# Kernel optimization log

Hardware: AMD Instinct MI355X
Metric: run time of the kernel (lower is better)

The kernel has to match this reference:

```python
import jax, jax.numpy as jnp
import numpy as np

N = 50000          # nodes
E = 800000         # edges (avg degree 16)
INPUT_DIM = 1024
K = 10             # conv1d kernel
STRIDE = 8
COUT = (INPUT_DIM - K) // STRIDE + 1   # 127, matches floor formula
H = 256            # hidden_dim


def setup_inputs() -> dict:
    key = jax.random.key(0)
    ks = jax.random.split(key, 12)
    sc = lambda k, s: (jax.random.normal(k, s, jnp.float32) * 0.05)
    inp = {}
    inp["h"] = jax.random.normal(ks[0], (N, INPUT_DIM), jnp.float32)
    inp["src"] = jax.random.randint(ks[1], (E,), 0, N, dtype=jnp.int32)
    inp["dst"] = jax.random.randint(ks[2], (E,), 0, N, dtype=jnp.int32)
    # Conv1d(1,1,k=10,stride=8)
    inp["conv1d_w"] = sc(ks[3], (1, 1, K))
    inp["conv1d_b"] = jnp.zeros((1,), jnp.float32)
    # SAGEConv1: 127 -> 256 (mean aggregator: fc_self + fc_neigh)
    inp["w_self1"] = sc(ks[4], (COUT, H))
    inp["w_neigh1"] = sc(ks[5], (COUT, H))
    inp["b1"] = jnp.zeros((H,), jnp.float32)
    # SAGEConv2: 256 -> 128
    inp["w_self2"] = sc(ks[6], (H, H // 2))
    inp["w_neigh2"] = sc(ks[7], (H, H // 2))
    inp["b2"] = jnp.zeros((H // 2,), jnp.float32)
    # MLP head 128 -> 64 -> 32 -> 1
    inp["fc1_w"] = sc(ks[8], (H // 2, H // 4)); inp["fc1_b"] = jnp.zeros((H // 4,), jnp.float32)
    inp["fc2_w"] = sc(ks[9], (H // 4, H // 8)); inp["fc2_b"] = jnp.zeros((H // 8,), jnp.float32)
    inp["fc3_w"] = sc(ks[10], (H // 8, 1));    inp["fc3_b"] = jnp.zeros((1,), jnp.float32)
    return inp


def _sage_mean(x, src, dst, w_self, w_neigh, b):
    # mean over in-neighbors (src -> dst), zero for isolated nodes (DGL semantics)
    ones = jnp.ones((src.shape[0],), x.dtype)
    deg = jax.ops.segment_sum(ones, dst, num_segments=N)          # [N]
    agg = jax.ops.segment_sum(x[src], dst, num_segments=N)        # [N, F]
    agg = agg / jnp.maximum(deg, 1.0)[:, None]
    return x @ w_self + agg @ w_neigh + b


def reference(h, src, dst, conv1d_w, conv1d_b,
              w_self1, w_neigh1, b1, w_self2, w_neigh2, b2,
              fc1_w, fc1_b, fc2_w, fc2_b, fc3_w, fc3_b):
    # per-node 1D conv over feature axis: [N,1,1024] -> [N,1,127]
    x = jax.lax.conv_general_dilated(h[:, None, :], conv1d_w, (STRIDE,), 'VALID',
                                     dimension_numbers=('NCH', 'OIH', 'NCH'))
    x = jax.nn.relu(x[:, 0, :] + conv1d_b)                        # [N, 127]
    x = jax.nn.relu(_sage_mean(x, src, dst, w_self1, w_neigh1, b1))  # [N, 256]
    x = jax.nn.relu(_sage_mean(x, src, dst, w_self2, w_neigh2, b2))  # [N, 128]
    hg = jnp.mean(x, axis=0, keepdims=True)                       # AvgPooling -> [1, 128]
    y = jax.nn.relu(hg @ fc1_w + fc1_b)
    y = jax.nn.relu(y @ fc2_w + fc2_b)
    return y @ fc3_w + fc3_b                                      # [1, 1]
```

## Files before the change

kernel.cpp:

```cpp
#include <hip/hip_runtime.h>

#define N_NODES 50000
#define N_EDGES 800000
#define IN_DIM  1024
#define COUT    127
#define H1      256
#define H2      128
#define LDA     256
#define MBLK    391
#define EPB     2048
#define NROWS   8192
#define LDSS    72
#define EBLK    782
#define CVB     256

typedef __bf16 bf16;
typedef __attribute__((ext_vector_type(8))) __bf16 bf16x8;
typedef __attribute__((ext_vector_type(2))) __bf16 bf16x2;
typedef __attribute__((ext_vector_type(4))) float floatx4;

__device__ __forceinline__ float blo(unsigned int u) { return __uint_as_float(u << 16); }
__device__ __forceinline__ float bhi(unsigned int u) { return __uint_as_float(u & 0xffff0000u); }

__device__ __forceinline__ void conv_range(const float* __restrict__ h,
                                           const float* __restrict__ w, float bb,
                                           bf16* __restrict__ xa,
                                           int lo, int hi, int cb, int ncb) {
    int t   = threadIdx.x & 127;
    int sub = threadIdx.x >> 7;
    float wv[10];
    #pragma unroll
    for (int j = 0; j < 10; ++j) wv[j] = w[j];
    for (int n = lo + cb * 8 + sub; n < hi; n += ncb * 8) {
        const float* hr = h + (size_t)n * IN_DIM;
        float r = 0.f;
        if (t < COUT) {
            const float* q = hr + t * 8;
            float4 a = *(const float4*)q;
            float4 c = *(const float4*)(q + 4);
            float2 d = *(const float2*)(q + 8);
            float s = bb;
            s += a.x * wv[0] + a.y * wv[1] + a.z * wv[2] + a.w * wv[3];
            s += c.x * wv[4] + c.y * wv[5] + c.z * wv[6] + c.w * wv[7];
            s += d.x * wv[8] + d.y * wv[9];
            r = fmaxf(s, 0.f);
        }
        xa[(size_t)n * LDA + t] = (bf16)r;
    }
}

__global__ void padw_kernel(const float* __restrict__ ws1, const float* __restrict__ wn1,
                            const float* __restrict__ ws2, const float* __restrict__ wn2,
                            bf16* __restrict__ wt1, bf16* __restrict__ wt2,
                            int* __restrict__ deg) {
    int i = blockIdx.x * blockDim.x + threadIdx.x;
    int j = i & 65535;
    int n = j >> 8, k = j & 255;
    if (i < 65536) {
        float v = 0.f;
        if (k < COUT)                        v = ws1[k * H1 + n];
        else if (k >= 128 && k < 128 + COUT) v = wn1[(k - 128) * H1 + n];
        wt1[j] = (bf16)v;
    } else {
        float v = (n < H2) ? ws2[k * H2 + n] : wn2[k * H2 + (n - H2)];
        wt2[j] = (bf16)v;
    }
    if (i < 50048) deg[i] = 0;
}

__global__ __launch_bounds__(1024) void deg_conv_kernel(
        const int* __restrict__ dst, int* __restrict__ deg,
        const float* __restrict__ h, const float* __restrict__ cw,
        const float* __restrict__ cb, bf16* __restrict__ xa) {
    int bid = blockIdx.x;
    if (bid < EBLK) {
        int e = bid * 1024 + threadIdx.x;
        if (e < N_EDGES) atomicAdd(&deg[dst[e]], 1);
    } else {
        conv_range(h, cw, cb[0], xa, 0, 25000, bid - EBLK, CVB);
    }
}

__device__ void scan_block(const int* __restrict__ deg, int* __restrict__ rowptr,
                           int* __restrict__ cursor) {
    __shared__ int wsum[16];
    __shared__ int carry_s;
    int tid = threadIdx.x;
    int lane = tid & 63, wid = tid >> 6;
    if (tid == 0) carry_s = 0;
    __syncthreads();
    for (int base = 0; base < N_NODES; base += 8192) {
        int i0 = base + tid * 8;
        int v[8];
        if (i0 + 8 <= N_NODES) {
            int4 a = *(const int4*)&deg[i0];
            int4 c = *(const int4*)&deg[i0 + 4];
            v[0] = a.x; v[1] = a.y; v[2] = a.z; v[3] = a.w;
            v[4] = c.x; v[5] = c.y; v[6] = c.z; v[7] = c.w;
        } else {
            #pragma unroll
            for (int j = 0; j < 8; ++j) v[j] = (i0 + j < N_NODES) ? deg[i0 + j] : 0;
        }
        int p[8]; int run = 0;
        #pragma unroll
        for (int j = 0; j < 8; ++j) { run += v[j]; p[j] = run; }
        int s = run;
        #pragma unroll
        for (int off = 1; off < 64; off <<= 1) {
            int t = __shfl_up(s, off);
            if (lane >= off) s += t;
        }
        if (lane == 63) wsum[wid] = s;
        __syncthreads();
        if (tid < 16) {
            int ws = wsum[tid];
            #pragma unroll
            for (int off = 1; off < 16; off <<= 1) {
                int t = __shfl_up(ws, off);
                if (tid >= off) ws += t;
            }
            wsum[tid] = ws;
        }
        __syncthreads();
        int wpre  = (wid == 0) ? 0 : wsum[wid - 1];
        int excl0 = carry_s + wpre + (s - run);
        int o[8];
        #pragma unroll
        for (int j = 0; j < 8; ++j) o[j] = excl0 + p[j] - v[j];
        if (i0 + 8 <= N_NODES) {
            *(int4*)&rowptr[i0]     = make_int4(o[0], o[1], o[2], o[3]);
            *(int4*)&rowptr[i0 + 4] = make_int4(o[4], o[5], o[6], o[7]);
            *(int4*)&cursor[i0]     = make_int4(o[0], o[1], o[2], o[3]);
            *(int4*)&cursor[i0 + 4] = make_int4(o[4], o[5], o[6], o[7]);
        } else {
            for (int j = 0; j < 8; ++j)
                if (i0 + j < N_NODES) { rowptr[i0 + j] = o[j]; cursor[i0 + j] = o[j]; }
        }
        int tot = wsum[15];
        __syncthreads();
        if (tid == 0) carry_s += tot;
        __syncthreads();
    }
    if (tid == 0) rowptr[N_NODES] = carry_s;
}

__global__ __launch_bounds__(1024) void scan_conv_kernel(
        const int* __restrict__ deg, int* __restrict__ rowptr, int* __restrict__ cursor,
        const float* __restrict__ h, const float* __restrict__ cw,
        const float* __restrict__ cb, bf16* __restrict__ xa) {
    if (blockIdx.x == 0) {
        scan_block(deg, rowptr, cursor);
    } else {
        conv_range(h, cw, cb[0], xa, 25000, N_NODES, blockIdx.x - 1, CVB);
    }
}

__global__ __launch_bounds__(1024) void fill_kernel(
        const int* __restrict__ src, const int* __restrict__ dst,
        int* __restrict__ cursor, int* __restrict__ esrc) {
    int e = blockIdx.x * 1024 + threadIdx.x;
    if (e < N_EDGES) {
        int d = dst[e];
        int pos = atomicAdd(&cursor[d], 1);
        esrc[pos] = src[e];
    }
}

__global__ __launch_bounds__(256) void agg_kernel(bf16* __restrict__ xa,
                                                  const int* __restrict__ rowptr,
                                                  const int* __restrict__ esrc) {
    int lane = threadIdx.x & 63;
    int w    = threadIdx.x >> 6;
    int n    = blockIdx.x * 4 + w;
    int s0 = __builtin_amdgcn_readfirstlane(rowptr[n]);
    int s1 = __builtin_amdgcn_readfirstlane(rowptr[n + 1]);
    float ax = 0.f, ay = 0.f;
    int e = s0;
    for (; e + 8 <= s1; e += 8) {
        int i0 = esrc[e],     i1 = esrc[e + 1], i2 = esrc[e + 2], i3 = esrc[e + 3];
        int i4 = esrc[e + 4], i5 = esrc[e + 5], i6 = esrc[e + 6], i7 = esrc[e + 7];
        unsigned u0 = ((const unsigned*)(xa + (size_t)i0 * LDA))[lane];
        unsigned u1 = ((const unsigned*)(xa + (size_t)i1 * LDA))[lane];
        unsigned u2 = ((const unsigned*)(xa + (size_t)i2 * LDA))[lane];
        unsigned u3 = ((const unsigned*)(xa + (size_t)i3 * LDA))[lane];
        unsigned u4 = ((const unsigned*)(xa + (size_t)i4 * LDA))[lane];
        unsigned u5 = ((const unsigned*)(xa + (size_t)i5 * LDA))[lane];
        unsigned u6 = ((const unsigned*)(xa + (size_t)i6 * LDA))[lane];
        unsigned u7 = ((const unsigned*)(xa + (size_t)i7 * LDA))[lane];
        ax += ((blo(u0) + blo(u1)) + (blo(u2) + blo(u3)))
            + ((blo(u4) + blo(u5)) + (blo(u6) + blo(u7)));
        ay += ((bhi(u0) + bhi(u1)) + (bhi(u2) + bhi(u3)))
            + ((bhi(u4) + bhi(u5)) + (bhi(u6) + bhi(u7)));
    }
    for (; e < s1; ++e) {
        unsigned u = ((const unsigned*)(xa + (size_t)esrc[e] * LDA))[lane];
        ax += blo(u); ay += bhi(u);
    }
    float dnm = (float)max(s1 - s0, 1);
    bf16x2 o;
    o[0] = (bf16)(ax / dnm);
    o[1] = (bf16)(ay / dnm);
    *(bf16x2*)(xa + (size_t)n * LDA + 128 + 2 * lane) = o;
}

template <bool RELU>
__global__ __launch_bounds__(256) void gemm_mfma(
        const bf16* __restrict__ X, const bf16* __restrict__ WT,
        const float* __restrict__ bias, bf16* __restrict__ out) {
    __shared__ bf16 As[128 * LDSS];
    __shared__ bf16 Bs[64 * LDSS];
    int tid  = threadIdx.x;
    int lane = tid & 63, w = tid >> 6;
    int quad = lane >> 4, l16 = lane & 15;
    int m0 = blockIdx.x * 128;
    int n0 = blockIdx.y * 64;
    floatx4 acc[2][4] = {};

    for (int k0 = 0; k0 < 256; k0 += 64) {
        uint4 av[4], bv[2];
        #pragma unroll
        for (int i = 0; i < 4; ++i) {
            int c = tid + 256 * i;
            int row = c >> 3, col = (c & 7) * 8;
            int gr = m0 + row;
            av[i] = (gr < N_NODES) ? *(const uint4*)(X + (size_t)gr * LDA + k0 + col)
                                   : make_uint4(0u, 0u, 0u, 0u);
        }
        #pragma unroll
        for (int i = 0; i < 2; ++i) {
            int c = tid + 256 * i;
            int row = c >> 3, col = (c & 7) * 8;
            bv[i] = *(const uint4*)(WT + (size_t)(n0 + row) * 256 + k0 + col);
        }
        __syncthreads();
        #pragma unroll
        for (int i = 0; i < 4; ++i) {
            int c = tid + 256 * i;
            int row = c >> 3, col = (c & 7) * 8;
            *(uint4*)&As[row * LDSS + col] = av[i];
        }
        #pragma unroll
        for (int i = 0; i < 2; ++i) {
            int c = tid + 256 * i;
            int row = c >> 3, col = (c & 7) * 8;
            *(uint4*)&Bs[row * LDSS + col] = bv[i];
        }
        __syncthreads();

        #pragma unroll
        for (int ks = 0; ks < 2; ++ks) {
            int kin = ks * 32 + quad * 8;
            bf16x8 a0 = *(const bf16x8*)&As[(w * 32 + l16) * LDSS + kin];
            bf16x8 a1 = *(const bf16x8*)&As[(w * 32 + 16 + l16) * LDSS + kin];
            bf16x8 b0 = *(const bf16x8*)&Bs[(l16) * LDSS + kin];
            bf16x8 b1 = *(const bf16x8*)&Bs[(16 + l16) * LDSS + kin];
            bf16x8 b2 = *(const bf16x8*)&Bs[(32 + l16) * LDSS + kin];
            bf16x8 b3 = *(const bf16x8*)&Bs[(48 + l16) * LDSS + kin];
            acc[0][0] = __builtin_amdgcn_mfma_f32_16x16x32_bf16(a0, b0, acc[0][0], 0, 0, 0);
            acc[0][1] = __builtin_amdgcn_mfma_f32_16x16x32_bf16(a0, b1, acc[0][1], 0, 0, 0);
            acc[0][2] = __builtin_amdgcn_mfma_f32_16x16x32_bf16(a0, b2, acc[0][2], 0, 0, 0);
            acc[0][3] = __builtin_amdgcn_mfma_f32_16x16x32_bf16(a0, b3, acc[0][3], 0, 0, 0);
            acc[1][0] = __builtin_amdgcn_mfma_f32_16x16x32_bf16(a1, b0, acc[1][0], 0, 0, 0);
            acc[1][1] = __builtin_amdgcn_mfma_f32_16x16x32_bf16(a1, b1, acc[1][1], 0, 0, 0);
            acc[1][2] = __builtin_amdgcn_mfma_f32_16x16x32_bf16(a1, b2, acc[1][2], 0, 0, 0);
            acc[1][3] = __builtin_amdgcn_mfma_f32_16x16x32_bf16(a1, b3, acc[1][3], 0, 0, 0);
        }
    }

    float bvv[4] = {};
    if constexpr (RELU) {
        #pragma unroll
        for (int nt = 0; nt < 4; ++nt) bvv[nt] = bias[n0 + nt * 16 + l16];
    }
    #pragma unroll
    for (int mt = 0; mt < 2; ++mt) {
        #pragma unroll
        for (int r = 0; r < 4; ++r) {
            int m = m0 + w * 32 + mt * 16 + quad * 4 + r;
            if (m < N_NODES) {
                #pragma unroll
                for (int nt = 0; nt < 4; ++nt) {
                    float v = acc[mt][nt][r];
                    if constexpr (RELU) v = fmaxf(v + bvv[nt], 0.f);
                    out[(size_t)m * LDA + n0 + nt * 16 + l16] = (bf16)v;
                }
            }
        }
    }
}

__global__ __launch_bounds__(256) void agg_epi_kernel(
        const bf16* __restrict__ P, const int* __restrict__ rowptr,
        const int* __restrict__ esrc, const float* __restrict__ b2,
        float* __restrict__ partial) {
    int lane = threadIdx.x & 63;
    int w    = threadIdx.x >> 6;
    int wid  = blockIdx.x * 4 + w;
    float2 bfv = *(const float2*)(b2 + 2 * lane);
    float csx = 0.f, csy = 0.f;
    for (int n = wid; n < N_NODES; n += 4 * gridDim.x) {
        int s0 = __builtin_amdgcn_readfirstlane(rowptr[n]);
        int s1 = __builtin_amdgcn_readfirstlane(rowptr[n + 1]);
        float ax = 0.f, ay = 0.f;
        int e = s0;
        for (; e + 8 <= s1; e += 8) {
            int i0 = esrc[e],     i1 = esrc[e + 1], i2 = esrc[e + 2], i3 = esrc[e + 3];
            int i4 = esrc[e + 4], i5 = esrc[e + 5], i6 = esrc[e + 6], i7 = esrc[e + 7];
            unsigned u0 = ((const unsigned*)(P + (size_t)i0 * LDA + H2))[lane];
            unsigned u1 = ((const unsigned*)(P + (size_t)i1 * LDA + H2))[lane];
            unsigned u2 = ((const unsigned*)(P + (size_t)i2 * LDA + H2))[lane];
            unsigned u3 = ((const unsigned*)(P + (size_t)i3 * LDA + H2))[lane];
            unsigned u4 = ((const unsigned*)(P + (size_t)i4 * LDA + H2))[lane];
            unsigned u5 = ((const unsigned*)(P + (size_t)i5 * LDA + H2))[lane];
            unsigned u6 = ((const unsigned*)(P + (size_t)i6 * LDA + H2))[lane];
            unsigned u7 = ((const unsigned*)(P + (size_t)i7 * LDA + H2))[lane];
            ax += ((blo(u0) + blo(u1)) + (blo(u2) + blo(u3)))
                + ((blo(u4) + blo(u5)) + (blo(u6) + blo(u7)));
            ay += ((bhi(u0) + bhi(u1)) + (bhi(u2) + bhi(u3)))
                + ((bhi(u4) + bhi(u5)) + (bhi(u6) + bhi(u7)));
        }
        for (; e < s1; ++e) {
            unsigned u = ((const unsigned*)(P + (size_t)esrc[e] * LDA + H2))[lane];
            ax += blo(u); ay += bhi(u);
        }
        float dnm = (float)max(s1 - s0, 1);
        unsigned us = ((const unsigned*)(P + (size_t)n * LDA))[lane];
        float yx = blo(us) + ax / dnm + bfv.x;
        float yy = bhi(us) + ay / dnm + bfv.y;
        csx += fmaxf(yx, 0.f);
        csy += fmaxf(yy, 0.f);
    }
    *(float2*)(partial + (size_t)wid * 128 + 2 * lane) = make_float2(csx, csy);
}

__global__ __launch_bounds__(256) void reduce_kernel(const float* __restrict__ partial,
                                                     float* __restrict__ hg) {
    int f = blockIdx.x, t = threadIdx.x;
    float s = 0.f;
    for (int i = t; i < NROWS; i += 256) s += partial[(size_t)i * 128 + f];
    __shared__ float ls[4];
    #pragma unroll
    for (int off = 32; off >= 1; off >>= 1) s += __shfl_down(s, off);
    if ((t & 63) == 0) ls[t >> 6] = s;
    __syncthreads();
    if (t == 0) hg[f] = (ls[0] + ls[1]) + (ls[2] + ls[3]);
}

__global__ void mlp_kernel(const float* __restrict__ hg,
                           const float* __restrict__ f1w, const float* __restrict__ f1b,
                           const float* __restrict__ f2w, const float* __restrict__ f2b,
                           const float* __restrict__ f3w, const float* __restrict__ f3b,
                           float* __restrict__ out) {
    __shared__ float h0[128], y1[64], y2[32];
    int t = threadIdx.x;
    if (t < 128) h0[t] = hg[t] * (1.0f / N_NODES);
    __syncthreads();
    if (t < 64) {
        float s = f1b[t];
        for (int k = 0; k < 128; ++k) s += h0[k] * f1w[k * 64 + t];
        y1[t] = fmaxf(s, 0.f);
    }
    __syncthreads();
    if (t < 32) {
        float s = f2b[t];
        for (int k = 0; k < 64; ++k) s += y1[k] * f2w[k * 32 + t];
        y2[t] = fmaxf(s, 0.f);
    }
    __syncthreads();
    if (t == 0) {
        float s = f3b[0];
        for (int k = 0; k < 32; ++k) s += y2[k] * f3w[k];
        out[0] = s;
    }
}

extern "C" void kernel_launch(void* const* d_in, const int* in_sizes, int n_in,
                              void* d_out, int out_size, void* d_ws, size_t ws_size,
                              hipStream_t stream) {
    (void)in_sizes; (void)n_in; (void)out_size; (void)ws_size;
    const float* h        = (const float*)d_in[0];
    const int*   src      = (const int*)d_in[1];
    const int*   dst      = (const int*)d_in[2];
    const float* cw       = (const float*)d_in[3];
    const float* cb       = (const float*)d_in[4];
    const float* w_self1  = (const float*)d_in[5];
    const float* w_neigh1 = (const float*)d_in[6];
    const float* b1       = (const float*)d_in[7];
    const float* w_self2  = (const float*)d_in[8];
    const float* w_neigh2 = (const float*)d_in[9];
    const float* b2       = (const float*)d_in[10];
    const float* f1w      = (const float*)d_in[11];
    const float* f1b      = (const float*)d_in[12];
    const float* f2w      = (const float*)d_in[13];
    const float* f2b      = (const float*)d_in[14];
    const float* f3w      = (const float*)d_in[15];
    const float* f3b      = (const float*)d_in[16];
    float* out = (float*)d_out;

    char* ws = (char*)d_ws;
    bf16*  xa    = (bf16*) (ws + 0);
    bf16*  P     = (bf16*) (ws + 0);
    bf16*  x2    = (bf16*) (ws + 25624576);
    bf16*  wt1   = (bf16*) (ws + 51249152);
    bf16*  wt2   = (bf16*) (ws + 51380224);
    int*   deg   = (int*)  (ws + 51511296);
    int*   rowp  = (int*)  (ws + 51711488);
    int*   esrc  = (int*)  (ws + 51911936);
    float* part  = (float*)(ws + 55111936);
    float* hg    = (float*)(ws + 59306240);
    int*   cur   = deg;

    padw_kernel<<<512, 256, 0, stream>>>(w_self1, w_neigh1, w_self2, w_neigh2, wt1, wt2, deg);
    deg_conv_kernel<<<EBLK + CVB, 1024, 0, stream>>>(dst, deg, h, cw, cb, xa);
    scan_conv_kernel<<<1 + CVB, 1024, 0, stream>>>(deg, rowp, cur, h, cw, cb, xa);
    fill_kernel<<<EBLK, 1024, 0, stream>>>(src, dst, cur, esrc);
    agg_kernel<<<12500, 256, 0, stream>>>(xa, rowp, esrc);
    dim3 g(MBLK, 4);
    gemm_mfma<true><<<g, 256, 0, stream>>>(xa, wt1, b1, x2);
    gemm_mfma<false><<<g, 256, 0, stream>>>(x2, wt2, nullptr, P);
    agg_epi_kernel<<<EPB, 256, 0, stream>>>(P, rowp, esrc, b2, part);
    reduce_kernel<<<128, 256, 0, stream>>>(part, hg);
    mlp_kernel<<<1, 128, 0, stream>>>(hg, f1w, f1b, f2w, f2b, f3w, f3b, out);
}
```

Baseline: 538.0 us.

## Fuse aggregation epilogue, global mean reduction and MLP head via last-block ticket

Merges the aggregation-epilogue, reduce and MLP kernels into one. Each block reduces its four wave partials in shared memory and atomically adds them into one of 64 slotted accumulators. An acquire-release ticket counter then picks the last block, which sums the slots and runs the tiny MLP. This removes two kernel launches and the large partial-buffer write and read, at the cost of float atomics, which make the summation order non-deterministic.

Result: slower. 584.6 us (+8.7%).

```diff
diff --git a/kernel.cpp b/kernel.cpp
--- a/kernel.cpp
+++ b/kernel.cpp
@@ -9,7 +9,7 @@
 #define LDA     256
 #define MBLK    391
 #define EPB     2048
-#define NROWS   8192
+#define NSLOT   64
 #define LDSS    72
 #define EBLK    782
 #define CVB     256
@@ -52,7 +52,8 @@
 __global__ void padw_kernel(const float* __restrict__ ws1, const float* __restrict__ wn1,
                             const float* __restrict__ ws2, const float* __restrict__ wn2,
                             bf16* __restrict__ wt1, bf16* __restrict__ wt2,
-                            int* __restrict__ deg) {
+                            int* __restrict__ deg, float* __restrict__ hgp,
+                            int* __restrict__ ticket) {
     int i = blockIdx.x * blockDim.x + threadIdx.x;
     int j = i & 65535;
     int n = j >> 8, k = j & 255;
@@ -66,6 +67,8 @@
         wt2[j] = (bf16)v;
     }
     if (i < 50048) deg[i] = 0;
+    if (i < NSLOT * 128) hgp[i] = 0.f;
+    if (i == 0) ticket[0] = 0;
 }
 
 __global__ __launch_bounds__(1024) void deg_conv_kernel(
@@ -289,16 +292,24 @@
     }
 }
 
-__global__ __launch_bounds__(256) void agg_epi_kernel(
+__global__ __launch_bounds__(256) void k7_agg_epi_mlp(
         const bf16* __restrict__ P, const int* __restrict__ rowptr,
         const int* __restrict__ esrc, const float* __restrict__ b2,
-        float* __restrict__ partial) {
-    int lane = threadIdx.x & 63;
-    int w    = threadIdx.x >> 6;
+        float* __restrict__ hgp, int* __restrict__ ticket,
+        const float* __restrict__ f1w, const float* __restrict__ f1b,
+        const float* __restrict__ f2w, const float* __restrict__ f2b,
+        const float* __restrict__ f3w, const float* __restrict__ f3b,
+        float* __restrict__ out) {
+    __shared__ float red[4][128];
+    __shared__ int last_s;
+    __shared__ float h0[128], y1[64], y2[32];
+    int tid  = threadIdx.x;
+    int lane = tid & 63;
+    int w    = tid >> 6;
     int wid  = blockIdx.x * 4 + w;
     float2 bfv = *(const float2*)(b2 + 2 * lane);
     float csx = 0.f, csy = 0.f;
-    for (int n = wid; n < N_NODES; n += 4 * gridDim.x) {
+    for (int n = wid; n < N_NODES; n += 4 * EPB) {
         int s0 = __builtin_amdgcn_readfirstlane(rowptr[n]);
         int s1 = __builtin_amdgcn_readfirstlane(rowptr[n + 1]);
         float ax = 0.f, ay = 0.f;
@@ -330,44 +341,45 @@
         csx += fmaxf(yx, 0.f);
         csy += fmaxf(yy, 0.f);
     }
-    *(float2*)(partial + (size_t)wid * 128 + 2 * lane) = make_float2(csx, csy);
-}
-
-__global__ __launch_bounds__(256) void reduce_kernel(const float* __restrict__ partial,
-                                                     float* __restrict__ hg) {
-    int f = blockIdx.x, t = threadIdx.x;
-    float s = 0.f;
-    for (int i = t; i < NROWS; i += 256) s += partial[(size_t)i * 128 + f];
-    __shared__ float ls[4];
-    #pragma unroll
-    for (int off = 32; off >= 1; off >>= 1) s += __shfl_down(s, off);
-    if ((t & 63) == 0) ls[t >> 6] = s;
-    __syncthreads();
-    if (t == 0) hg[f] = (ls[0] + ls[1]) + (ls[2] + ls[3]);
-}
-
-__global__ void mlp_kernel(const float* __restrict__ hg,
-                           const float* __restrict__ f1w, const float* __restrict__ f1b,
-                           const float* __restrict__ f2w, const float* __restrict__ f2b,
-                           const float* __restrict__ f3w, const float* __restrict__ f3b,
-                           float* __restrict__ out) {
-    __shared__ float h0[128], y1[64], y2[32];
-    int t = threadIdx.x;
-    if (t < 128) h0[t] = hg[t] * (1.0f / N_NODES);
-    __syncthreads();
-    if (t < 64) {
-        float s = f1b[t];
-        for (int k = 0; k < 128; ++k) s += h0[k] * f1w[k * 64 + t];
-        y1[t] = fmaxf(s, 0.f);
-    }
-    __syncthreads();
-    if (t < 32) {
-        float s = f2b[t];
-        for (int k = 0; k < 64; ++k) s += y1[k] * f2w[k * 32 + t];
-        y2[t] = fmaxf(s, 0.f);
-    }
-    __syncthreads();
-    if (t == 0) {
+    red[w][2 * lane]     = csx;
+    red[w][2 * lane + 1] = csy;
+    __syncthreads();
+    int slot = blockIdx.x & (NSLOT - 1);
+    if (tid < 128) {
+        float s = (red[0][tid] + red[1][tid]) + (red[2][tid] + red[3][tid]);
+        atomicAdd(&hgp[slot * 128 + tid], s);
+    }
+    __syncthreads();
+    if (tid == 0) {
+        int t0 = __hip_atomic_fetch_add(ticket, 1, __ATOMIC_ACQ_REL,
+                                        __HIP_MEMORY_SCOPE_AGENT);
+        last_s = (t0 == EPB - 1);
+    }
+    __syncthreads();
+    if (!last_s) return;
+
+    if (tid < 128) {
+        float s = 0.f;
+        #pragma unroll 8
+        for (int sl = 0; sl < NSLOT; ++sl)
+            s += __hip_atomic_load(&hgp[sl * 128 + tid], __ATOMIC_RELAXED,
+                                   __HIP_MEMORY_SCOPE_AGENT);
+        h0[tid] = s * (1.0f / N_NODES);
+    }
+    __syncthreads();
+    if (tid < 64) {
+        float s = f1b[tid];
+        for (int k = 0; k < 128; ++k) s += h0[k] * f1w[k * 64 + tid];
+        y1[tid] = fmaxf(s, 0.f);
+    }
+    __syncthreads();
+    if (tid < 32) {
+        float s = f2b[tid];
+        for (int k = 0; k < 64; ++k) s += y1[k] * f2w[k * 32 + tid];
+        y2[tid] = fmaxf(s, 0.f);
+    }
+    __syncthreads();
+    if (tid == 0) {
         float s = f3b[0];
         for (int k = 0; k < 32; ++k) s += y2[k] * f3w[k];
         out[0] = s;
@@ -406,11 +418,12 @@
     int*   deg   = (int*)  (ws + 51511296);
     int*   rowp  = (int*)  (ws + 51711488);
     int*   esrc  = (int*)  (ws + 51911936);
-    float* part  = (float*)(ws + 55111936);
-    float* hg    = (float*)(ws + 59306240);
+    float* hgp   = (float*)(ws + 55111936);
+    int*   tick  = (int*)  (ws + 55144704);
     int*   cur   = deg;
 
-    padw_kernel<<<512, 256, 0, stream>>>(w_self1, w_neigh1, w_self2, w_neigh2, wt1, wt2, deg);
+    padw_kernel<<<512, 256, 0, stream>>>(w_self1, w_neigh1, w_self2, w_neigh2,
+                                         wt1, wt2, deg, hgp, tick);
     deg_conv_kernel<<<EBLK + CVB, 1024, 0, stream>>>(dst, deg, h, cw, cb, xa);
     scan_conv_kernel<<<1 + CVB, 1024, 0, stream>>>(deg, rowp, cur, h, cw, cb, xa);
     fill_kernel<<<EBLK, 1024, 0, stream>>>(src, dst, cur, esrc);
@@ -418,7 +431,6 @@
     dim3 g(MBLK, 4);
     gemm_mfma<true><<<g, 256, 0, stream>>>(xa, wt1, b1, x2);
     gemm_mfma<false><<<g, 256, 0, stream>>>(x2, wt2, nullptr, P);
-    agg_epi_kernel<<<EPB, 256, 0, stream>>>(P, rowp, esrc, b2, part);
-    reduce_kernel<<<128, 256, 0, stream>>>(part, hg);
-    mlp_kernel<<<1, 128, 0, stream>>>(hg, f1w, f1b, f2w, f2b, f3w, f3b, out);
-}
+    k7_agg_epi_mlp<<<EPB, 256, 0, stream>>>(P, rowp, esrc, b2, hgp, tick,
+                                            f1w, f1b, f2w, f2b, f3w, f3b, out);
+}
```

## Use direct global-to-LDS loads with XOR swizzle in GEMM; split-wave gather aggregation

Applied to the files above, without the earlier changes.

The GEMM now loads A and B tiles with global_load_lds 16-byte transfers into unpadded 64-wide LDS tiles, using an XOR swizzle to avoid bank conflicts. This replaces the register staging and padded layout. Both aggregation kernels now split each wave into two halves that fetch different neighbor rows with 8-byte loads and combine them with a cross-half shuffle, so each load instruction has more gathers in flight. The risks are lower per-lane load width, the extra shuffle and reduction work, and the correctness of clamping out-of-range rows in the GEMM.

After: 517.9 us. 1.04x faster.

```diff
diff --git a/kernel.cpp b/kernel.cpp
--- a/kernel.cpp
+++ b/kernel.cpp
@@ -10,17 +10,22 @@
 #define MBLK    391
 #define EPB     2048
 #define NROWS   8192
-#define LDSS    72
 #define EBLK    782
 #define CVB     256
 
 typedef __bf16 bf16;
 typedef __attribute__((ext_vector_type(8))) __bf16 bf16x8;
-typedef __attribute__((ext_vector_type(2))) __bf16 bf16x2;
+typedef __attribute__((ext_vector_type(4))) __bf16 bf16x4;
 typedef __attribute__((ext_vector_type(4))) float floatx4;
 
 __device__ __forceinline__ float blo(unsigned int u) { return __uint_as_float(u << 16); }
 __device__ __forceinline__ float bhi(unsigned int u) { return __uint_as_float(u & 0xffff0000u); }
+
+__device__ __forceinline__ void gload16(const void* g, void* l) {
+    __builtin_amdgcn_global_load_lds(
+        (const __attribute__((address_space(1))) unsigned int*)g,
+        (__attribute__((address_space(3))) unsigned int*)l, 16, 0, 0);
+}
 
 __device__ __forceinline__ void conv_range(const float* __restrict__ h,
                                            const float* __restrict__ w, float bb,
@@ -171,44 +176,56 @@
                                                   const int* __restrict__ esrc) {
     int lane = threadIdx.x & 63;
     int w    = threadIdx.x >> 6;
+    int half = lane >> 5;
+    int l32  = lane & 31;
     int n    = blockIdx.x * 4 + w;
     int s0 = __builtin_amdgcn_readfirstlane(rowptr[n]);
     int s1 = __builtin_amdgcn_readfirstlane(rowptr[n + 1]);
-    float ax = 0.f, ay = 0.f;
+    float a0 = 0.f, a1 = 0.f, a2 = 0.f, a3 = 0.f;
     int e = s0;
     for (; e + 8 <= s1; e += 8) {
-        int i0 = esrc[e],     i1 = esrc[e + 1], i2 = esrc[e + 2], i3 = esrc[e + 3];
-        int i4 = esrc[e + 4], i5 = esrc[e + 5], i6 = esrc[e + 6], i7 = esrc[e + 7];
-        unsigned u0 = ((const unsigned*)(xa + (size_t)i0 * LDA))[lane];
-        unsigned u1 = ((const unsigned*)(xa + (size_t)i1 * LDA))[lane];
-        unsigned u2 = ((const unsigned*)(xa + (size_t)i2 * LDA))[lane];
-        unsigned u3 = ((const unsigned*)(xa + (size_t)i3 * LDA))[lane];
-        unsigned u4 = ((const unsigned*)(xa + (size_t)i4 * LDA))[lane];
-        unsigned u5 = ((const unsigned*)(xa + (size_t)i5 * LDA))[lane];
-        unsigned u6 = ((const unsigned*)(xa + (size_t)i6 * LDA))[lane];
-        unsigned u7 = ((const unsigned*)(xa + (size_t)i7 * LDA))[lane];
-        ax += ((blo(u0) + blo(u1)) + (blo(u2) + blo(u3)))
-            + ((blo(u4) + blo(u5)) + (blo(u6) + blo(u7)));
-        ay += ((bhi(u0) + bhi(u1)) + (bhi(u2) + bhi(u3)))
-            + ((bhi(u4) + bhi(u5)) + (bhi(u6) + bhi(u7)));
-    }
-    for (; e < s1; ++e) {
-        unsigned u = ((const unsigned*)(xa + (size_t)esrc[e] * LDA))[lane];
-        ax += blo(u); ay += bhi(u);
-    }
-    float dnm = (float)max(s1 - s0, 1);
-    bf16x2 o;
-    o[0] = (bf16)(ax / dnm);
-    o[1] = (bf16)(ay / dnm);
-    *(bf16x2*)(xa + (size_t)n * LDA + 128 + 2 * lane) = o;
+        int i0 = esrc[e     + half];
+        int i1 = esrc[e + 2 + half];
+        int i2 = esrc[e + 4 + half];
+        int i3 = esrc[e + 6 + half];
+        uint2 u0 = ((const uint2*)(xa + (size_t)i0 * LDA))[l32];
+        uint2 u1 = ((const uint2*)(xa + (size_t)i1 * LDA))[l32];
+        uint2 u2 = ((const uint2*)(xa + (size_t)i2 * LDA))[l32];
+        uint2 u3 = ((const uint2*)(xa + (size_t)i3 * LDA))[l32];
+        a0 += (blo(u0.x) + blo(u1.x)) + (blo(u2.x) + blo(u3.x));
+        a1 += (bhi(u0.x) + bhi(u1.x)) + (bhi(u2.x) + bhi(u3.x));
+        a2 += (blo(u0.y) + blo(u1.y)) + (blo(u2.y) + blo(u3.y));
+        a3 += (bhi(u0.y) + bhi(u1.y)) + (bhi(u2.y) + bhi(u3.y));
+    }
+    for (; e + 2 <= s1; e += 2) {
+        int i = esrc[e + half];
+        uint2 u = ((const uint2*)(xa + (size_t)i * LDA))[l32];
+        a0 += blo(u.x); a1 += bhi(u.x); a2 += blo(u.y); a3 += bhi(u.y);
+    }
+    if (e < s1) {
+        int i = esrc[e];
+        uint2 u = ((const uint2*)(xa + (size_t)i * LDA))[l32];
+        if (half == 0) { a0 += blo(u.x); a1 += bhi(u.x); a2 += blo(u.y); a3 += bhi(u.y); }
+    }
+    a0 += __shfl_xor(a0, 32);
+    a1 += __shfl_xor(a1, 32);
+    a2 += __shfl_xor(a2, 32);
+    a3 += __shfl_xor(a3, 32);
+    if (half == 0) {
+        float dnm = (float)max(s1 - s0, 1);
+        bf16x4 o;
+        o[0] = (bf16)(a0 / dnm); o[1] = (bf16)(a1 / dnm);
+        o[2] = (bf16)(a2 / dnm); o[3] = (bf16)(a3 / dnm);
+        *(bf16x4*)(xa + (size_t)n * LDA + 128 + l32 * 4) = o;
+    }
 }
 
 template <bool RELU>
 __global__ __launch_bounds__(256) void gemm_mfma(
         const bf16* __restrict__ X, const bf16* __restrict__ WT,
         const float* __restrict__ bias, bf16* __restrict__ out) {
-    __shared__ bf16 As[128 * LDSS];
-    __shared__ bf16 Bs[64 * LDSS];
+    __shared__ bf16 As[128 * 64];
+    __shared__ bf16 Bs[64 * 64];
     int tid  = threadIdx.x;
     int lane = tid & 63, w = tid >> 6;
     int quad = lane >> 4, l16 = lane & 15;
@@ -217,45 +234,33 @@
     floatx4 acc[2][4] = {};
 
     for (int k0 = 0; k0 < 256; k0 += 64) {
-        uint4 av[4], bv[2];
-        #pragma unroll
-        for (int i = 0; i < 4; ++i) {
-            int c = tid + 256 * i;
-            int row = c >> 3, col = (c & 7) * 8;
-            int gr = m0 + row;
-            av[i] = (gr < N_NODES) ? *(const uint4*)(X + (size_t)gr * LDA + k0 + col)
-                                   : make_uint4(0u, 0u, 0u, 0u);
-        }
-        #pragma unroll
-        for (int i = 0; i < 2; ++i) {
-            int c = tid + 256 * i;
-            int row = c >> 3, col = (c & 7) * 8;
-            bv[i] = *(const uint4*)(WT + (size_t)(n0 + row) * 256 + k0 + col);
-        }
-        __syncthreads();
-        #pragma unroll
-        for (int i = 0; i < 4; ++i) {
-            int c = tid + 256 * i;
-            int row = c >> 3, col = (c & 7) * 8;
-            *(uint4*)&As[row * LDSS + col] = av[i];
-        }
-        #pragma unroll
-        for (int i = 0; i < 2; ++i) {
-            int c = tid + 256 * i;
-            int row = c >> 3, col = (c & 7) * 8;
-            *(uint4*)&Bs[row * LDSS + col] = bv[i];
+        __syncthreads();
+        #pragma unroll
+        for (int j = 0; j < 4; ++j) {
+            int C = (w * 4 + j) * 64 + lane;
+            int r = C >> 3, cp = C & 7;
+            int c = cp ^ (r & 7);
+            int gr = min(m0 + r, N_NODES - 1);
+            gload16(X + (size_t)gr * LDA + k0 + c * 8, &As[(w * 4 + j) * 512]);
+        }
+        #pragma unroll
+        for (int j = 0; j < 2; ++j) {
+            int C = (w * 2 + j) * 64 + lane;
+            int r = C >> 3, cp = C & 7;
+            int c = cp ^ (r & 7);
+            gload16(WT + (size_t)(n0 + r) * 256 + k0 + c * 8, &Bs[(w * 2 + j) * 512]);
         }
         __syncthreads();
 
         #pragma unroll
         for (int ks = 0; ks < 2; ++ks) {
-            int kin = ks * 32 + quad * 8;
-            bf16x8 a0 = *(const bf16x8*)&As[(w * 32 + l16) * LDSS + kin];
-            bf16x8 a1 = *(const bf16x8*)&As[(w * 32 + 16 + l16) * LDSS + kin];
-            bf16x8 b0 = *(const bf16x8*)&Bs[(l16) * LDSS + kin];
-            bf16x8 b1 = *(const bf16x8*)&Bs[(16 + l16) * LDSS + kin];
-            bf16x8 b2 = *(const bf16x8*)&Bs[(32 + l16) * LDSS + kin];
-            bf16x8 b3 = *(const bf16x8*)&Bs[(48 + l16) * LDSS + kin];
+            int cs = ((ks * 4 + quad) ^ (l16 & 7)) * 8;
+            bf16x8 a0 = *(const bf16x8*)&As[(w * 32 + l16) * 64 + cs];
+            bf16x8 a1 = *(const bf16x8*)&As[(w * 32 + 16 + l16) * 64 + cs];
+            bf16x8 b0 = *(const bf16x8*)&Bs[(l16) * 64 + cs];
+            bf16x8 b1 = *(const bf16x8*)&Bs[(16 + l16) * 64 + cs];
+            bf16x8 b2 = *(const bf16x8*)&Bs[(32 + l16) * 64 + cs];
+            bf16x8 b3 = *(const bf16x8*)&Bs[(48 + l16) * 64 + cs];
             acc[0][0] = __builtin_amdgcn_mfma_f32_16x16x32_bf16(a0, b0, acc[0][0], 0, 0, 0);
             acc[0][1] = __builtin_amdgcn_mfma_f32_16x16x32_bf16(a0, b1, acc[0][1], 0, 0, 0);
             acc[0][2] = __builtin_amdgcn_mfma_f32_16x16x32_bf16(a0, b2, acc[0][2], 0, 0, 0);
@@ -295,42 +300,55 @@
         float* __restrict__ partial) {
     int lane = threadIdx.x & 63;
     int w    = threadIdx.x >> 6;
+    int half = lane >> 5;
+    int l32  = lane & 31;
     int wid  = blockIdx.x * 4 + w;
-    float2 bfv = *(const float2*)(b2 + 2 * lane);
-    float csx = 0.f, csy = 0.f;
-    for (int n = wid; n < N_NODES; n += 4 * gridDim.x) {
+    float4 bfv = ((const float4*)b2)[l32];
+    float cs0 = 0.f, cs1 = 0.f, cs2 = 0.f, cs3 = 0.f;
+    for (int n = wid; n < N_NODES; n += 4 * EPB) {
         int s0 = __builtin_amdgcn_readfirstlane(rowptr[n]);
         int s1 = __builtin_amdgcn_readfirstlane(rowptr[n + 1]);
-        float ax = 0.f, ay = 0.f;
+        float a0 = 0.f, a1 = 0.f, a2 = 0.f, a3 = 0.f;
         int e = s0;
         for (; e + 8 <= s1; e += 8) {
-            int i0 = esrc[e],     i1 = esrc[e + 1], i2 = esrc[e + 2], i3 = esrc[e + 3];
-            int i4 = esrc[e + 4], i5 = esrc[e + 5], i6 = esrc[e + 6], i7 = esrc[e + 7];
-            unsigned u0 = ((const unsigned*)(P + (size_t)i0 * LDA + H2))[lane];
-            unsigned u1 = ((const unsigned*)(P + (size_t)i1 * LDA + H2))[lane];
-            unsigned u2 = ((const unsigned*)(P + (size_t)i2 * LDA + H2))[lane];
-            unsigned u3 = ((const unsigned*)(P + (size_t)i3 * LDA + H2))[lane];
-            unsigned u4 = ((const unsigned*)(P + (size_t)i4 * LDA + H2))[lane];
-            unsigned u5 = ((const unsigned*)(P + (size_t)i5 * LDA + H2))[lane];
-            unsigned u6 = ((const unsigned*)(P + (size_t)i6 * LDA + H2))[lane];
-            unsigned u7 = ((const unsigned*)(P + (size_t)i7 * LDA + H2))[lane];
-            ax += ((blo(u0) + blo(u1)) + (blo(u2) + blo(u3)))
-                + ((blo(u4) + blo(u5)) + (blo(u6) + blo(u7)));
-            ay += ((bhi(u0) + bhi(u1)) + (bhi(u2) + bhi(u3)))
-                + ((bhi(u4) + bhi(u5)) + (bhi(u6) + bhi(u7)));
-        }
-        for (; e < s1; ++e) {
-            unsigned u = ((const unsigned*)(P + (size_t)esrc[e] * LDA + H2))[lane];
-            ax += blo(u); ay += bhi(u);
-        }
-        float dnm = (float)max(s1 - s0, 1);
-        unsigned us = ((const unsigned*)(P + (size_t)n * LDA))[lane];
-        float yx = blo(us) + ax / dnm + bfv.x;
-        float yy = bhi(us) + ay / dnm + bfv.y;
-        csx += fmaxf(yx, 0.f);
-        csy += fmaxf(yy, 0.f);
-    }
-    *(float2*)(partial + (size_t)wid * 128 + 2 * lane) = make_float2(csx, csy);
+            int i0 = esrc[e     + half];
+            int i1 = esrc[e + 2 + half];
+            int i2 = esrc[e + 4 + half];
+            int i3 = esrc[e + 6 + half];
+            uint2 u0 = ((const uint2*)(P + (size_t)i0 * LDA + H2))[l32];
+            uint2 u1 = ((const uint2*)(P + (size_t)i1 * LDA + H2))[l32];
+            uint2 u2 = ((const uint2*)(P + (size_t)i2 * LDA + H2))[l32];
+            uint2 u3 = ((const uint2*)(P + (size_t)i3 * LDA + H2))[l32];
+            a0 += (blo(u0.x) + blo(u1.x)) + (blo(u2.x) + blo(u3.x));
+            a1 += (bhi(u0.x) + bhi(u1.x)) + (bhi(u2.x) + bhi(u3.x));
+            a2 += (blo(u0.y) + blo(u1.y)) + (blo(u2.y) + blo(u3.y));
+            a3 += (bhi(u0.y) + bhi(u1.y)) + (bhi(u2.y) + bhi(u3.y));
+        }
+        for (; e + 2 <= s1; e += 2) {
+            int i = esrc[e + half];
+            uint2 u = ((const uint2*)(P + (size_t)i * LDA + H2))[l32];
+            a0 += blo(u.x); a1 += bhi(u.x); a2 += blo(u.y); a3 += bhi(u.y);
+        }
+        if (e < s1) {
+            int i = esrc[e];
+            uint2 u = ((const uint2*)(P + (size_t)i * LDA + H2))[l32];
+            if (half == 0) { a0 += blo(u.x); a1 += bhi(u.x); a2 += blo(u.y); a3 += bhi(u.y); }
+        }
+        a0 += __shfl_xor(a0, 32);
+        a1 += __shfl_xor(a1, 32);
+        a2 += __shfl_xor(a2, 32);
+        a3 += __shfl_xor(a3, 32);
+        uint2 us = ((const uint2*)(P + (size_t)n * LDA))[l32];
+        if (half == 0) {
+            float dnm = (float)max(s1 - s0, 1);
+            cs0 += fmaxf(blo(us.x) + a0 / dnm + bfv.x, 0.f);
+            cs1 += fmaxf(bhi(us.x) + a1 / dnm + bfv.y, 0.f);
+            cs2 += fmaxf(blo(us.y) + a2 / dnm + bfv.z, 0.f);
+            cs3 += fmaxf(bhi(us.y) + a3 / dnm + bfv.w, 0.f);
+        }
+    }
+    if (half == 0)
+        *(float4*)(partial + (size_t)wid * 128 + l32 * 4) = make_float4(cs0, cs1, cs2, cs3);
 }
 
 __global__ __launch_bounds__(256) void reduce_kernel(const float* __restrict__ partial,
```
